# Kernel optimization log

Measured on AMD Instinct MI355X. Metric: run time of the kernel, lower is better.

The kernel has to match this reference:

```python
import jax, jax.numpy as jnp
import numpy as np

LT_INDICES = np.array([[0, 1, 3], [1, 2, 4], [3, 4, 5]])  # lower-triangle -> 3x3
SYMEIG_EPS = 1e-6  # noise scale used by SymEig
N_GRADS = 64
B_VALUE = 1000.0


def _design_matrix(n_grads=N_GRADS, b=B_VALUE, seed=0):
    """dipy.reconst.dti.design_matrix equivalent: columns Dxx,Dxy,Dyy,Dxz,Dyz,Dzz, dummy; returns -B."""
    rng = np.random.default_rng(seed)
    g = rng.normal(size=(n_grads, 3))
    g /= np.linalg.norm(g, axis=1, keepdims=True)
    B = np.empty((n_grads, 7), dtype=np.float64)
    B[:, 0] = g[:, 0] * g[:, 0] * b
    B[:, 1] = g[:, 0] * g[:, 1] * 2.0 * b
    B[:, 2] = g[:, 1] * g[:, 1] * b
    B[:, 3] = g[:, 0] * g[:, 2] * 2.0 * b
    B[:, 4] = g[:, 1] * g[:, 2] * 2.0 * b
    B[:, 5] = g[:, 2] * g[:, 2] * b
    B[:, 6] = 1.0
    return -B


def setup_inputs() -> dict:
    key = jax.random.key(0)
    k1, _ = jax.random.split(key)
    D = _design_matrix()
    design_matrix_inv = jnp.asarray(np.linalg.pinv(D), dtype=jnp.float32)  # [7, n_grads]
    min_diffusivity = jnp.asarray(1e-6 / -D.min(), dtype=jnp.float32)
    dwi = jax.random.uniform(k1, (100, 100, 100, N_GRADS), dtype=jnp.float32)
    mask = jnp.ones((100, 100, 100, 1), dtype=jnp.float32)
    return {"dwi": dwi, "mask": mask, "design_matrix_inv": design_matrix_inv,
            "min_diffusivity": min_diffusivity}


def reference(dwi, mask, design_matrix_inv, min_diffusivity):
    # WLS log-linear DTI fit
    dwi = jnp.maximum(dwi, min_diffusivity)
    fit = jnp.einsum('ij,...j->...i', design_matrix_inv, jnp.log(dwi))  # [...,7]
    tensors = fit[..., LT_INDICES]  # [...,3,3] symmetric diffusion tensors
    # SymEig: add tiny gaussian noise (degeneracy breaking), re-symmetrize
    noise = SYMEIG_EPS * jax.random.normal(jax.random.key(42), tensors.shape, dtype=tensors.dtype)
    t = tensors + noise
    t = (t + jnp.swapaxes(t, -1, -2)) * 0.5
    eigenvals, eigenvectors = jnp.linalg.eigh(t)  # [...,3], [...,3,3]
    eigenvals = jnp.maximum(eigenvals, min_diffusivity)
    eigenvals = jnp.where(jnp.isnan(eigenvals), 0.0, eigenvals)
    all_zero = jnp.all(eigenvals == 0, axis=-1).astype(eigenvals.dtype)
    ev1, ev2, ev3 = eigenvals[..., 0], eigenvals[..., 1], eigenvals[..., 2]
    num = 0.5 * ((ev1 - ev2) ** 2 + (ev2 - ev3) ** 2 + (ev3 - ev1) ** 2)
    den = jnp.sum(eigenvals * eigenvals, axis=-1) + all_zero
    fa = jnp.sqrt(num / den)[..., None]  # [...,1]
    return fa * mask
```

## Files before the change

### kernel.cpp

```cpp
#include <hip/hip_runtime.h>


__device__ __forceinline__ unsigned tf_rotl(unsigned x, int r) {
  return (x << r) | (x >> (32 - r));
}

__device__ __forceinline__ unsigned threefry_second(unsigned x0, unsigned x1) {
  const unsigned k0 = 0u, k1 = 42u;
  const unsigned k2 = 0x1BD11BDAu ^ k0 ^ k1;
  x0 += k0; x1 += k1;
#define TF_ROUND(r) { x0 += x1; x1 = tf_rotl(x1, r); x1 ^= x0; }
  TF_ROUND(13) TF_ROUND(15) TF_ROUND(26) TF_ROUND(6)
  x0 += k1; x1 += k2 + 1u;
  TF_ROUND(17) TF_ROUND(29) TF_ROUND(16) TF_ROUND(24)
  x0 += k2; x1 += k0 + 2u;
  TF_ROUND(13) TF_ROUND(15) TF_ROUND(26) TF_ROUND(6)
  x0 += k0; x1 += k1 + 3u;
  TF_ROUND(17) TF_ROUND(29) TF_ROUND(16) TF_ROUND(24)
  x0 += k1; x1 += k2 + 4u;
  TF_ROUND(13) TF_ROUND(15) TF_ROUND(26) TF_ROUND(6)
  x0 += k2; x1 += k0 + 5u;
#undef TF_ROUND
  (void)x0;
  return x1;
}

__device__ __forceinline__ float erfinv_xla(float x) {
  float w = -__logf(fmaf(-x, x, 1.0f));
  float p;
  if (w < 5.0f) {
    w = w - 2.5f;
    p = 2.81022636e-08f;
    p = fmaf(p, w, 3.43273939e-07f);
    p = fmaf(p, w, -3.5233877e-06f);
    p = fmaf(p, w, -4.39150654e-06f);
    p = fmaf(p, w, 0.00021858087f);
    p = fmaf(p, w, -0.00125372503f);
    p = fmaf(p, w, -0.00417768164f);
    p = fmaf(p, w, 0.246640727f);
    p = fmaf(p, w, 1.50140941f);
  } else {
    w = __builtin_sqrtf(w) - 3.0f;
    p = -0.000200214257f;
    p = fmaf(p, w, 0.000100950558f);
    p = fmaf(p, w, 0.00134934322f);
    p = fmaf(p, w, -0.00367342844f);
    p = fmaf(p, w, 0.00573950773f);
    p = fmaf(p, w, -0.0076224613f);
    p = fmaf(p, w, 0.00943887047f);
    p = fmaf(p, w, 1.00167406f);
    p = fmaf(p, w, 2.83297682f);
  }
  return p * x;
}

__device__ __forceinline__ float jax_normal_at(unsigned idx) {
  unsigned bits = threefry_second(0u, idx);
  float f = __uint_as_float((bits >> 9) | 0x3F800000u);
  float u = f - 1.0f;
  const float lo = -0.99999994f;
  float val = fmaf(u, 2.0f, lo);
  val = fmaxf(lo, val);
  return 1.41421356237f * erfinv_xla(val);
}

#define NG 64

__global__ __launch_bounds__(256) void fa_kernel(
    const float* __restrict__ dwi,
    const float* __restrict__ mask,
    const float* __restrict__ W,
    const float* __restrict__ mdp,
    float* __restrict__ out,
    int nvox)
{
  int v = blockIdx.x * 256 + threadIdx.x;
  if (v >= nvox) return;
  const float md = mdp[0];

  const float4* __restrict__ p =
      reinterpret_cast<const float4*>(dwi + (size_t)v * NG);
  float f0 = 0.f, f1 = 0.f, f2 = 0.f, f3 = 0.f, f4 = 0.f, f5 = 0.f;
#pragma unroll
  for (int j4 = 0; j4 < NG / 4; ++j4) {
    float4 d = p[j4];
    float xs[4];
    xs[0] = __logf(fmaxf(d.x, md));
    xs[1] = __logf(fmaxf(d.y, md));
    xs[2] = __logf(fmaxf(d.z, md));
    xs[3] = __logf(fmaxf(d.w, md));
#pragma unroll
    for (int k = 0; k < 4; ++k) {
      int j = j4 * 4 + k;
      float x = xs[k];
      f0 = fmaf(W[0 * NG + j], x, f0);
      f1 = fmaf(W[1 * NG + j], x, f1);
      f2 = fmaf(W[2 * NG + j], x, f2);
      f3 = fmaf(W[3 * NG + j], x, f3);
      f4 = fmaf(W[4 * NG + j], x, f4);
      f5 = fmaf(W[5 * NG + j], x, f5);
    }
  }

  unsigned base = 9u * (unsigned)v;
  float z[9];
#pragma unroll
  for (int e = 0; e < 9; ++e) z[e] = jax_normal_at(base + (unsigned)e);

  const float eps = 1e-6f;
  float a00 = f0 + eps * z[0];
  float a11 = f2 + eps * z[4];
  float a22 = f5 + eps * z[8];
  float a01 = ((f1 + eps * z[1]) + (f1 + eps * z[3])) * 0.5f;
  float a02 = ((f3 + eps * z[2]) + (f3 + eps * z[6])) * 0.5f;
  float a12 = ((f4 + eps * z[5]) + (f4 + eps * z[7])) * 0.5f;

  float q = (a00 + a11 + a22) * (1.0f / 3.0f);
  float aa = a00 - q, bb = a11 - q, cc = a22 - q;
  float p2 = aa * aa + bb * bb + cc * cc +
             2.0f * (a01 * a01 + a02 * a02 + a12 * a12);
  float pp = __builtin_sqrtf(p2 * (1.0f / 6.0f));
  float invp = (pp > 0.0f) ? (1.0f / pp) : 0.0f;
  float b00 = aa * invp, b11 = bb * invp, b22 = cc * invp;
  float b01 = a01 * invp, b02 = a02 * invp, b12 = a12 * invp;
  float detB = b00 * (b11 * b22 - b12 * b12)
             - b01 * (b01 * b22 - b12 * b02)
             + b02 * (b01 * b12 - b11 * b02);
  float r = 0.5f * detB;
  r = fminf(1.0f, fmaxf(-1.0f, r));
  float phi = acosf(r) * (1.0f / 3.0f);
  float l0 = q + 2.0f * pp * cosf(phi);
  float l2 = q + 2.0f * pp * cosf(phi + 2.0943951023931953f);
  float l1 = 3.0f * q - l0 - l2;

  l0 = fmaxf(l0, md);
  l1 = fmaxf(l1, md);
  l2 = fmaxf(l2, md);
  float d01 = l0 - l1, d12 = l1 - l2, d20 = l2 - l0;
  float num = 0.5f * (d01 * d01 + d12 * d12 + d20 * d20);
  float den = l0 * l0 + l1 * l1 + l2 * l2;
  float fa = __builtin_sqrtf(num / den);

  out[v] = fa * mask[v];
}

extern "C" void kernel_launch(void* const* d_in, const int* in_sizes, int n_in,
                              void* d_out, int out_size, void* d_ws, size_t ws_size,
                              hipStream_t stream) {
  const float* dwi  = (const float*)d_in[0];
  const float* mask = (const float*)d_in[1];
  const float* W    = (const float*)d_in[2];
  const float* mdp  = (const float*)d_in[3];
  float* out = (float*)d_out;
  int nvox = in_sizes[0] / NG;
  int grid = (nvox + 255) / 256;
  hipLaunchKernelGGL(fa_kernel, dim3(grid), dim3(256), 0, stream,
                     dwi, mask, W, mdp, out, nvox);
}
```

Baseline: 359.4 us.

## Stage DWI loads through LDS with coalesced chunked loads and register prefetch

Before, each thread read its own 256-byte voxel row with strided float4 loads, so accesses within a wavefront were uncoalesced. Now the block loads 16-gradient chunks cooperatively, with four consecutive threads covering one voxel's chunk. It transposes them through padded shared memory (stride 17) and prefetches the next chunk into registers while computing the current one. The cost is two barriers per chunk, LDS traffic, and about 17KB of shared memory per block, which may limit occupancy.

```diff
diff --git a/kernel.cpp b/kernel.cpp
--- a/kernel.cpp
+++ b/kernel.cpp
@@ -65,8 +65,12 @@
 }
 
 #define NG 64
+#define BLK 256
+#define CH 16
+#define NC (NG / CH)
+#define LSTRIDE 17
 
-__global__ __launch_bounds__(256) void fa_kernel(
+__global__ __launch_bounds__(BLK) void fa_kernel(
     const float* __restrict__ dwi,
     const float* __restrict__ mask,
     const float* __restrict__ W,
@@ -74,25 +78,54 @@
     float* __restrict__ out,
     int nvox)
 {
-  int v = blockIdx.x * 256 + threadIdx.x;
-  if (v >= nvox) return;
+  __shared__ float lds[BLK * LSTRIDE];
+
+  const int tid = threadIdx.x;
+  const int v0 = blockIdx.x * BLK;
   const float md = mdp[0];
 
-  const float4* __restrict__ p =
-      reinterpret_cast<const float4*>(dwi + (size_t)v * NG);
   float f0 = 0.f, f1 = 0.f, f2 = 0.f, f3 = 0.f, f4 = 0.f, f5 = 0.f;
+
+  float4 buf[4];
 #pragma unroll
-  for (int j4 = 0; j4 < NG / 4; ++j4) {
-    float4 d = p[j4];
-    float xs[4];
-    xs[0] = __logf(fmaxf(d.x, md));
-    xs[1] = __logf(fmaxf(d.y, md));
-    xs[2] = __logf(fmaxf(d.z, md));
-    xs[3] = __logf(fmaxf(d.w, md));
+  for (int i = 0; i < 4; ++i) {
+    int idx4 = tid + BLK * i;
+    int vv = idx4 >> 2, q = idx4 & 3;
+    int gv = v0 + vv; if (gv >= nvox) gv = nvox - 1;
+    buf[i] = reinterpret_cast<const float4*>(
+        dwi + (size_t)gv * NG + 0 * CH)[q];
+  }
+
 #pragma unroll
-    for (int k = 0; k < 4; ++k) {
-      int j = j4 * 4 + k;
-      float x = xs[k];
+  for (int c = 0; c < NC; ++c) {
+#pragma unroll
+    for (int i = 0; i < 4; ++i) {
+      int idx4 = tid + BLK * i;
+      int vv = idx4 >> 2, q = idx4 & 3;
+      int s = vv * LSTRIDE + q * 4;
+      lds[s + 0] = buf[i].x;
+      lds[s + 1] = buf[i].y;
+      lds[s + 2] = buf[i].z;
+      lds[s + 3] = buf[i].w;
+    }
+    __syncthreads();
+
+    if (c < NC - 1) {
+#pragma unroll
+      for (int i = 0; i < 4; ++i) {
+        int idx4 = tid + BLK * i;
+        int vv = idx4 >> 2, q = idx4 & 3;
+        int gv = v0 + vv; if (gv >= nvox) gv = nvox - 1;
+        buf[i] = reinterpret_cast<const float4*>(
+            dwi + (size_t)gv * NG + (c + 1) * CH)[q];
+      }
+    }
+
+    const int lb = tid * LSTRIDE;
+#pragma unroll
+    for (int k = 0; k < CH; ++k) {
+      float x = __logf(fmaxf(lds[lb + k], md));
+      int j = c * CH + k;
       f0 = fmaf(W[0 * NG + j], x, f0);
       f1 = fmaf(W[1 * NG + j], x, f1);
       f2 = fmaf(W[2 * NG + j], x, f2);
@@ -100,7 +133,11 @@
       f4 = fmaf(W[4 * NG + j], x, f4);
       f5 = fmaf(W[5 * NG + j], x, f5);
     }
+    __syncthreads();
   }
+
+  const int v = v0 + tid;
+  if (v >= nvox) return;
 
   unsigned base = 9u * (unsigned)v;
   float z[9];
@@ -153,7 +190,7 @@
   const float* mdp  = (const float*)d_in[3];
   float* out = (float*)d_out;
   int nvox = in_sizes[0] / NG;
-  int grid = (nvox + 255) / 256;
-  hipLaunchKernelGGL(fa_kernel, dim3(grid), dim3(256), 0, stream,
+  int grid = (nvox + BLK - 1) / BLK;
+  hipLaunchKernelGGL(fa_kernel, dim3(grid), dim3(BLK), 0, stream,
                      dwi, mask, W, mdp, out, nvox);
 }
```

Result: slower. 371.5 us (+3.4%).
